# Performance work log

Measured on AMD Instinct MI355X. Metric: run time of the kernel, lower is better.

The kernel has to match this reference:

```python
import jax, jax.numpy as jnp
import numpy as np
import math

N_HEADS = 16
THETA = 10000.0


def setup_inputs() -> dict:
    key = jax.random.key(0)
    ks = jax.random.split(key, 5)
    B, T, D = 4, 2048, 1024
    return {
        "x": jax.random.normal(ks[0], (B, T, D), dtype=jnp.float32),
        "w_qkv": jax.random.normal(ks[1], (3 * D, D), dtype=jnp.float32) * 0.02,
        "b_qkv": jax.random.normal(ks[2], (3 * D,), dtype=jnp.float32) * 0.02,
        "w_out": jax.random.normal(ks[3], (D, D), dtype=jnp.float32) * 0.02,
        "b_out": jax.random.normal(ks[4], (D,), dtype=jnp.float32) * 0.02,
    }


def reference(x, w_qkv, b_qkv, w_out, b_out):
    B, T, D = x.shape
    H = N_HEADS
    hd = D // H
    half = hd // 2

    # fused QKV projection (nn.Linear: y = x @ W^T + b)
    qkv = (x @ w_qkv.T + b_qkv).reshape(B, T, 3, H, hd)
    q, k, v = qkv[:, :, 0], qkv[:, :, 1], qkv[:, :, 2]

    # RoPE: interleaved (even, odd) pairs treated as complex, rotated by e^{i t w}
    inv_freq = 1.0 / (THETA ** (jnp.arange(0, hd, 2, dtype=jnp.float32) / hd))  # [half]
    angles = jnp.arange(T, dtype=jnp.float32)[:, None] * inv_freq[None, :]      # [T, half]
    cos = jnp.cos(angles)[None, :, None, :]  # [1,T,1,half]
    sin = jnp.sin(angles)[None, :, None, :]

    def rotate(t):
        tr = t.reshape(B, T, H, half, 2)
        te, to = tr[..., 0], tr[..., 1]
        rot = jnp.stack([te * cos - to * sin, te * sin + to * cos], axis=-1)
        return rot.reshape(B, T, H, hd).astype(t.dtype)

    q, k = rotate(q), rotate(k)

    # non-causal SDPA, scale = 1/sqrt(head_dim)
    scale = 1.0 / math.sqrt(hd)
    scores = jnp.einsum("bqhd,bkhd->bhqk", q, k) * scale
    attn = jax.nn.softmax(scores, axis=-1)
    out = jnp.einsum("bhqk,bkhd->bqhd", attn, v).reshape(B, T, D)

    return out @ w_out.T + b_out
```

## Files before the change

### kernel.cpp

```cpp
#include <hip/hip_runtime.h>

typedef __attribute__((ext_vector_type(4))) float f32x4;
typedef __attribute__((ext_vector_type(16))) float f32x16;
typedef __attribute__((ext_vector_type(8))) short bf16x8;
typedef __attribute__((ext_vector_type(4))) unsigned u32x4;

__device__ __forceinline__ unsigned short f2bf(float f) {
  unsigned u = __float_as_uint(f);
  u += 0x7fff + ((u >> 16) & 1);
  return (unsigned short)(u >> 16);
}
__device__ __forceinline__ float bf2f(unsigned short h) {
  return __uint_as_float(((unsigned)h) << 16);
}

__device__ __forceinline__ void gload_lds16(const void* g, void* lds) {
  __builtin_amdgcn_global_load_lds(
      (const __attribute__((address_space(1))) unsigned int*)g,
      (__attribute__((address_space(3))) unsigned int*)lds, 16, 0, 0);
}

__global__ void cast_f32_bf16(const float* __restrict__ in,
                              unsigned short* __restrict__ out, int n4) {
  int i = blockIdx.x * blockDim.x + threadIdx.x;
  if (i >= n4) return;
  float4 v = ((const float4*)in)[i];
  ushort4 o;
  o.x = f2bf(v.x); o.y = f2bf(v.y); o.z = f2bf(v.z); o.w = f2bf(v.w);
  ((ushort4*)out)[i] = o;
}

__global__ void rope_table(float2* __restrict__ cs) {
  int idx = blockIdx.x * blockDim.x + threadIdx.x;
  if (idx >= 2048 * 32) return;
  int t = idx >> 5, i = idx & 31;
  float inv = powf(10000.0f, -(float)(2 * i) / 64.0f);
  float a = (float)t * inv;
  cs[idx] = make_float2(cosf(a), sinf(a));
}

__global__ void rope_apply_k(unsigned short* __restrict__ qkv,
                             const float2* __restrict__ cs) {
  int idx = blockIdx.x * blockDim.x + threadIdx.x;
  int i = idx & 31;
  int h = (idx >> 5) & 15;
  int t = (idx >> 9) & 2047;
  int b = idx >> 20;
  float2 v = cs[(t << 5) | i];
  unsigned short* p =
      qkv + ((size_t)((b << 11) + t)) * 3072 + 1024 + h * 64 + 2 * i;
  unsigned pr = *(unsigned*)p;
  float e = bf2f((unsigned short)(pr & 0xffff));
  float o = bf2f((unsigned short)(pr >> 16));
  float ne = e * v.x - o * v.y;
  float no = e * v.y + o * v.x;
  *(unsigned*)p = (unsigned)f2bf(ne) | ((unsigned)f2bf(no) << 16);
}

template <int OUT_BF16>
__global__ __launch_bounds__(256, 2) void gemm_bt(
    const unsigned short* __restrict__ A, const unsigned short* __restrict__ B,
    const float* __restrict__ bias, void* __restrict__ Cout,
    int M, int N, int K) {
  __shared__ unsigned short lA[128 * 64];
  __shared__ unsigned short lB[128 * 64];
  const int tiles_n = N >> 7;
  const int swz = (blockIdx.x & 7) * (gridDim.x >> 3) + (blockIdx.x >> 3);
  const int bm = swz / tiles_n;
  const int bn = swz % tiles_n;
  const int tid = threadIdx.x;
  const int w = tid >> 6, l = tid & 63;
  const int l15 = l & 15, lq = l >> 4;
  const int wm = (w >> 1) * 64, wn = (w & 1) * 64;
  const int m0 = bm << 7, n0 = bn << 7;
  const int arow = l >> 3;
  const int acol = (l & 7) * 8;
  f32x4 acc[4][4] = {};

  for (int k0 = 0; k0 < K; k0 += 64) {
    __syncthreads();
#pragma unroll
    for (int it = 0; it < 4; ++it) {
      const int rb = it * 32 + w * 8;
      gload_lds16(A + (size_t)(m0 + rb + arow) * K + k0 + acol, &lA[rb * 64]);
      gload_lds16(B + (size_t)(n0 + rb + arow) * K + k0 + acol, &lB[rb * 64]);
    }
    __syncthreads();
#pragma unroll
    for (int ks = 0; ks < 2; ++ks) {
      bf16x8 af[4], bfr[4];
#pragma unroll
      for (int mi = 0; mi < 4; ++mi)
        af[mi] = *(const bf16x8*)&lA[(wm + mi * 16 + l15) * 64 + ks * 32 + lq * 8];
#pragma unroll
      for (int ni = 0; ni < 4; ++ni)
        bfr[ni] = *(const bf16x8*)&lB[(wn + ni * 16 + l15) * 64 + ks * 32 + lq * 8];
#pragma unroll
      for (int mi = 0; mi < 4; ++mi)
#pragma unroll
        for (int ni = 0; ni < 4; ++ni)
          acc[mi][ni] = __builtin_amdgcn_mfma_f32_16x16x32_bf16(
              af[mi], bfr[ni], acc[mi][ni], 0, 0, 0);
    }
  }

#pragma unroll
  for (int ni = 0; ni < 4; ++ni) {
    const int c = n0 + wn + ni * 16 + l15;
    const float bv = bias[c];
#pragma unroll
    for (int mi = 0; mi < 4; ++mi) {
#pragma unroll
      for (int j = 0; j < 4; ++j) {
        const int r = m0 + wm + mi * 16 + lq * 4 + j;
        const float v = acc[mi][ni][j] + bv;
        if (OUT_BF16)
          ((unsigned short*)Cout)[(size_t)r * N + c] = f2bf(v);
        else
          ((float*)Cout)[(size_t)r * N + c] = v;
      }
    }
  }
}


#define PACKPV(SCV, KS)                                                        \
  do {                                                                         \
    unsigned xa, xb, ya, yb;                                                   \
    asm("v_cvt_pk_bf16_f32 %0, %1, %2"                                         \
        : "=v"(xa) : "v"(SCV[((KS) & 1) * 8 + 0]), "v"(SCV[((KS) & 1) * 8 + 1])); \
    asm("v_cvt_pk_bf16_f32 %0, %1, %2"                                         \
        : "=v"(xb) : "v"(SCV[((KS) & 1) * 8 + 2]), "v"(SCV[((KS) & 1) * 8 + 3])); \
    asm("v_cvt_pk_bf16_f32 %0, %1, %2"                                         \
        : "=v"(ya) : "v"(SCV[((KS) & 1) * 8 + 4]), "v"(SCV[((KS) & 1) * 8 + 5])); \
    asm("v_cvt_pk_bf16_f32 %0, %1, %2"                                         \
        : "=v"(yb) : "v"(SCV[((KS) & 1) * 8 + 6]), "v"(SCV[((KS) & 1) * 8 + 7])); \
    asm("v_permlane32_swap_b32 %0, %1" : "+v"(xa), "+v"(ya));                  \
    asm("v_permlane32_swap_b32 %0, %1" : "+v"(xb), "+v"(yb));                  \
    u32x4 pw;                                                                  \
    pw[0] = xa; pw[1] = xb; pw[2] = ya; pw[3] = yb;                            \
    const bf16x8 pa = __builtin_bit_cast(bf16x8, pw);                          \
    {                                                                          \
      const bf16x8 vf = *(const bf16x8*)                                       \
          &lVc[l31 * 136 + ((16 * (KS) + 8 * hi) ^ (l31 & 0x30))];             \
      o0 = __builtin_amdgcn_mfma_f32_32x32x16_bf16(pa, vf, o0, 0, 0, 0);       \
    }                                                                          \
    {                                                                          \
      const int vrow = 32 + l31;                                               \
      const bf16x8 vf = *(const bf16x8*)                                       \
          &lVc[vrow * 136 + ((16 * (KS) + 8 * hi) ^ (vrow & 0x30))];           \
      o1 = __builtin_amdgcn_mfma_f32_32x32x16_bf16(pa, vf, o1, 0, 0, 0);       \
    }                                                                          \
  } while (0)

__global__ __launch_bounds__(256, 2) void attn_fwd(
    const unsigned short* __restrict__ qkv, unsigned short* __restrict__ aout,
    const float2* __restrict__ cs) {
  __shared__ unsigned short lK[2 * 128 * 64];
  __shared__ unsigned short lVt[2 * 64 * 136];

  const int g = blockIdx.x;
  const int xcd = g & 7;
  const int j2 = g >> 3;
  const int bh = ((j2 >> 4) << 3) + xcd;
  const int qt = j2 & 15;
  const int h = bh & 15, b = bh >> 4;

  const int tid = threadIdx.x;
  const int w = tid >> 6, l = tid & 63;
  const int l31 = l & 31, hi = l >> 5;
  const int l7 = l & 7;

  const size_t bt_base = (size_t)(b * 2048) * 3072;
  const int qbase = qt * 128 + w * 32;

  const unsigned short* Qp =
      qkv + bt_base + (size_t)(qbase + l31) * 3072 + h * 64 + hi * 8;
  const float2* csrow = cs + (size_t)(qbase + l31) * 32;
  bf16x8 qf[4];
#pragma unroll
  for (int s = 0; s < 4; ++s) {
    bf16x8 q = *(const bf16x8*)(Qp + 16 * s);
#pragma unroll
    for (int j = 0; j < 4; ++j) {
      const float2 cn = csrow[8 * s + 4 * hi + j];
      const float e = bf2f((unsigned short)q[2 * j]);
      const float o = bf2f((unsigned short)q[2 * j + 1]);
      q[2 * j]     = (short)f2bf((e * cn.x - o * cn.y) * 0.125f);
      q[2 * j + 1] = (short)f2bf((e * cn.y + o * cn.x) * 0.125f);
    }
    qf[s] = q;
  }

  const unsigned short* Kp = qkv + bt_base + 1024 + h * 64;
  const unsigned short* Vp = qkv + bt_base + 2048 + h * 64;

  const int krow = l >> 3;
  const int kcol = ((l & 7) ^ (l >> 3)) << 3;

  const int vr = tid >> 2;
  const int vc0 = (tid & 3) << 4;

  f32x16 o0 = {}, o1 = {};
  float m_run = -1e30f, lsum = 0.f;
  bf16x8 v0, v1, v2, v3;
  const float L2E = 1.4426950408889634f;

  {
#pragma unroll
    for (int it = 0; it < 4; ++it) {
      const int rb = it * 32 + w * 8;
      gload_lds16(Kp + (size_t)(rb + krow) * 3072 + kcol, &lK[rb * 64]);
    }
    const unsigned short* vb = Vp + (size_t)vr * 3072 + vc0;
    v0 = *(const bf16x8*)vb;
    v1 = *(const bf16x8*)(vb + 8);
    const unsigned short* vb2 = vb + (size_t)64 * 3072;
    v2 = *(const bf16x8*)vb2;
    v3 = *(const bf16x8*)(vb2 + 8);
#pragma unroll
    for (int i2 = 0; i2 < 8; ++i2) {
      lVt[(vc0 + i2) * 136 + (vr ^ vc0)] = (unsigned short)v0[i2];
      lVt[(vc0 + 8 + i2) * 136 + (vr ^ vc0)] = (unsigned short)v1[i2];
      lVt[(vc0 + i2) * 136 + ((vr + 64) ^ vc0)] = (unsigned short)v2[i2];
      lVt[(vc0 + 8 + i2) * 136 + ((vr + 64) ^ vc0)] = (unsigned short)v3[i2];
    }
  }
  __syncthreads();

  for (int t = 0; t < 16; ++t) {
    const int cur = t & 1;
    const unsigned short* lKc = lK + cur * 8192;
    const unsigned short* lVc = lVt + cur * 8704;

    if (t < 15) {
      const unsigned short* kb = Kp + (size_t)(t + 1) * 128 * 3072;
      unsigned short* lKn = lK + (cur ^ 1) * 8192;
#pragma unroll
      for (int it = 0; it < 4; ++it) {
        const int rb = it * 32 + w * 8;
        gload_lds16(kb + (size_t)(rb + krow) * 3072 + kcol, lKn + rb * 64);
      }
      const unsigned short* vb =
          Vp + (size_t)(t + 1) * 128 * 3072 + (size_t)vr * 3072 + vc0;
      v0 = *(const bf16x8*)vb;
      v1 = *(const bf16x8*)(vb + 8);
      const unsigned short* vb2 = vb + (size_t)64 * 3072;
      v2 = *(const bf16x8*)vb2;
      v3 = *(const bf16x8*)(vb2 + 8);
    }

    f32x16 s0 = {}, s1 = {}, s2 = {}, s3 = {};
    __builtin_amdgcn_s_setprio(1);
#pragma unroll
    for (int s = 0; s < 4; ++s) {
      bf16x8 kf = *(const bf16x8*)&lKc[l31 * 64 + (((2 * s + hi) ^ l7) << 3)];
      s0 = __builtin_amdgcn_mfma_f32_32x32x16_bf16(kf, qf[s], s0, 0, 0, 0);
    }
#pragma unroll
    for (int s = 0; s < 4; ++s) {
      bf16x8 kf = *(const bf16x8*)&lKc[(32 + l31) * 64 + (((2 * s + hi) ^ l7) << 3)];
      s1 = __builtin_amdgcn_mfma_f32_32x32x16_bf16(kf, qf[s], s1, 0, 0, 0);
    }
#pragma unroll
    for (int s = 0; s < 4; ++s) {
      bf16x8 kf = *(const bf16x8*)&lKc[(64 + l31) * 64 + (((2 * s + hi) ^ l7) << 3)];
      s2 = __builtin_amdgcn_mfma_f32_32x32x16_bf16(kf, qf[s], s2, 0, 0, 0);
    }
#pragma unroll
    for (int s = 0; s < 4; ++s) {
      bf16x8 kf = *(const bf16x8*)&lKc[(96 + l31) * 64 + (((2 * s + hi) ^ l7) << 3)];
      s3 = __builtin_amdgcn_mfma_f32_32x32x16_bf16(kf, qf[s], s3, 0, 0, 0);
    }
    __builtin_amdgcn_s_setprio(0);

    {
      float pmax = -1e30f;
#pragma unroll
      for (int r = 0; r < 16; r += 2) {
        float t0, t1, t2, t3;
        asm("v_max3_f32 %0, %1, %2, %3"
            : "=v"(t0) : "v"(s0[r]), "v"(s0[r + 1]), "v"(pmax));
        asm("v_max3_f32 %0, %1, %2, %3"
            : "=v"(t1) : "v"(s1[r]), "v"(s1[r + 1]), "v"(t0));
        asm("v_max3_f32 %0, %1, %2, %3"
            : "=v"(t2) : "v"(s2[r]), "v"(s2[r + 1]), "v"(t1));
        asm("v_max3_f32 %0, %1, %2, %3"
            : "=v"(t3) : "v"(s3[r]), "v"(s3[r + 1]), "v"(t2));
        pmax = t3;
      }
      pmax = fmaxf(pmax, __shfl_xor(pmax, 32));
      if (!__all(pmax <= m_run + 8.0f)) {
        const float mn = fmaxf(m_run, pmax);
        const float alpha = __expf(m_run - mn);
        m_run = mn;
        lsum *= alpha;
#pragma unroll
        for (int r = 0; r < 16; ++r) {
          const float ar = __shfl(alpha, (r & 3) + 8 * (r >> 2) + 4 * hi);
          o0[r] *= ar;
          o1[r] *= ar;
        }
      }
      const float m2 = m_run * L2E;
      float rsa = 0.f, rsb = 0.f;
#pragma unroll
      for (int r = 0; r < 16; r += 2) {
        float a0 = __builtin_fmaf(s0[r], L2E, -m2);
        float a1 = __builtin_fmaf(s0[r + 1], L2E, -m2);
        float p0, p1;
        asm("v_exp_f32 %0, %1" : "=v"(p0) : "v"(a0));
        asm("v_exp_f32 %0, %1" : "=v"(p1) : "v"(a1));
        s0[r] = p0; s0[r + 1] = p1; rsa += p0; rsb += p1;
        a0 = __builtin_fmaf(s1[r], L2E, -m2);
        a1 = __builtin_fmaf(s1[r + 1], L2E, -m2);
        asm("v_exp_f32 %0, %1" : "=v"(p0) : "v"(a0));
        asm("v_exp_f32 %0, %1" : "=v"(p1) : "v"(a1));
        s1[r] = p0; s1[r + 1] = p1; rsa += p0; rsb += p1;
        a0 = __builtin_fmaf(s2[r], L2E, -m2);
        a1 = __builtin_fmaf(s2[r + 1], L2E, -m2);
        asm("v_exp_f32 %0, %1" : "=v"(p0) : "v"(a0));
        asm("v_exp_f32 %0, %1" : "=v"(p1) : "v"(a1));
        s2[r] = p0; s2[r + 1] = p1; rsa += p0; rsb += p1;
        a0 = __builtin_fmaf(s3[r], L2E, -m2);
        a1 = __builtin_fmaf(s3[r + 1], L2E, -m2);
        asm("v_exp_f32 %0, %1" : "=v"(p0) : "v"(a0));
        asm("v_exp_f32 %0, %1" : "=v"(p1) : "v"(a1));
        s3[r] = p0; s3[r + 1] = p1; rsa += p0; rsb += p1;
      }
      float rs = rsa + rsb;
      rs += __shfl_xor(rs, 32);
      lsum += rs;
    }

    __builtin_amdgcn_s_setprio(1);
    PACKPV(s0, 0);
    PACKPV(s0, 1);
    PACKPV(s1, 2);
    PACKPV(s1, 3);
    PACKPV(s2, 4);
    PACKPV(s2, 5);
    PACKPV(s3, 6);
    PACKPV(s3, 7);
    __builtin_amdgcn_s_setprio(0);

    if (t < 15) {
      unsigned short* lVn = lVt + (cur ^ 1) * 8704;
#pragma unroll
      for (int i2 = 0; i2 < 8; ++i2) {
        lVn[(vc0 + i2) * 136 + (vr ^ vc0)] = (unsigned short)v0[i2];
        lVn[(vc0 + 8 + i2) * 136 + (vr ^ vc0)] = (unsigned short)v1[i2];
        lVn[(vc0 + i2) * 136 + ((vr + 64) ^ vc0)] = (unsigned short)v2[i2];
        lVn[(vc0 + 8 + i2) * 136 + ((vr + 64) ^ vc0)] = (unsigned short)v3[i2];
      }
    }
    __syncthreads();
  }

  const float linv = 1.0f / lsum;
#pragma unroll
  for (int r = 0; r < 16; ++r) {
    const int crow = (r & 3) + 8 * (r >> 2) + 4 * hi;
    const float lr = __shfl(linv, crow);
    unsigned short* orow =
        aout + (size_t)(b * 2048 + qbase + crow) * 1024 + h * 64 + l31;
    orow[0] = f2bf(o0[r] * lr);
    orow[32] = f2bf(o1[r] * lr);
  }
}

extern "C" void kernel_launch(void* const* d_in, const int* in_sizes, int n_in,
                              void* d_out, int out_size, void* d_ws, size_t ws_size,
                              hipStream_t stream) {
  const float* x     = (const float*)d_in[0];
  const float* w_qkv = (const float*)d_in[1];
  const float* b_qkv = (const float*)d_in[2];
  const float* w_out = (const float*)d_in[3];
  const float* b_out = (const float*)d_in[4];
  float* out = (float*)d_out;

  char* ws = (char*)d_ws;
  unsigned short* x_bf    = (unsigned short*)(ws);
  unsigned short* wqkv_bf = (unsigned short*)(ws + 16777216);
  unsigned short* wout_bf = (unsigned short*)(ws + 23068672);
  unsigned short* qkv     = (unsigned short*)(ws + 25165824);
  unsigned short* aout    = (unsigned short*)(ws + 75497472);
  float2* cs              = (float2*)(ws + 92274688);

  cast_f32_bf16<<<2097152 / 256, 256, 0, stream>>>(x, x_bf, 2097152);
  cast_f32_bf16<<<786432 / 256, 256, 0, stream>>>(w_qkv, wqkv_bf, 786432);
  cast_f32_bf16<<<262144 / 256, 256, 0, stream>>>(w_out, wout_bf, 262144);
  rope_table<<<65536 / 256, 256, 0, stream>>>(cs);

  gemm_bt<1><<<64 * 24, 256, 0, stream>>>(x_bf, wqkv_bf, b_qkv, qkv,
                                          8192, 3072, 1024);
  rope_apply_k<<<4194304 / 256, 256, 0, stream>>>(qkv, cs);
  attn_fwd<<<1024, 256, 0, stream>>>(qkv, aout, cs);
  gemm_bt<0><<<64 * 8, 256, 0, stream>>>(aout, wout_bf, b_out, out,
                                         8192, 1024, 1024);
}
```

Baseline: 219.9 us.

## Use 512-thread attention blocks with 64-key tiles; fuse three cast kernels

The attention kernel now runs 8 waves per block over 256 query rows and iterates over 64-key K/V tiles (32 iterations) instead of 4 waves with 128-key tiles. This halves the LDS footprint per block and doubles the number of waves sharing each K/V tile, aiming for more reuse and occupancy. The cost is twice as many barriers and a shorter compute span per iteration to hide the next tile's loads behind. Separately, the three f32-to-bf16 cast launches are merged into one kernel that branches on index range, removing two launches.

```diff
diff --git a/kernel.cpp b/kernel.cpp
--- a/kernel.cpp
+++ b/kernel.cpp
@@ -20,14 +20,23 @@
       (__attribute__((address_space(3))) unsigned int*)lds, 16, 0, 0);
 }
 
-__global__ void cast_f32_bf16(const float* __restrict__ in,
-                              unsigned short* __restrict__ out, int n4) {
+__global__ void cast3_f32_bf16(const float* __restrict__ x,
+                               const float* __restrict__ wq,
+                               const float* __restrict__ wo,
+                               unsigned short* __restrict__ xb,
+                               unsigned short* __restrict__ wqb,
+                               unsigned short* __restrict__ wob) {
   int i = blockIdx.x * blockDim.x + threadIdx.x;
-  if (i >= n4) return;
-  float4 v = ((const float4*)in)[i];
+  const float* src;
+  unsigned short* dst;
+  int off;
+  if (i < 2097152) { src = x;  dst = xb;  off = i; }
+  else if (i < 2883584) { src = wq; dst = wqb; off = i - 2097152; }
+  else { src = wo; dst = wob; off = i - 2883584; }
+  float4 v = ((const float4*)src)[off];
   ushort4 o;
   o.x = f2bf(v.x); o.y = f2bf(v.y); o.z = f2bf(v.z); o.w = f2bf(v.w);
-  ((ushort4*)out)[i] = o;
+  ((ushort4*)dst)[off] = o;
 }
 
 __global__ void rope_table(float2* __restrict__ cs) {
@@ -142,28 +151,28 @@
     const bf16x8 pa = __builtin_bit_cast(bf16x8, pw);                          \
     {                                                                          \
       const bf16x8 vf = *(const bf16x8*)                                       \
-          &lVc[l31 * 136 + ((16 * (KS) + 8 * hi) ^ (l31 & 0x30))];             \
+          &lVc[l31 * 72 + ((16 * (KS) + 8 * hi) ^ (l31 & 0x30))];              \
       o0 = __builtin_amdgcn_mfma_f32_32x32x16_bf16(pa, vf, o0, 0, 0, 0);       \
     }                                                                          \
     {                                                                          \
       const int vrow = 32 + l31;                                               \
       const bf16x8 vf = *(const bf16x8*)                                       \
-          &lVc[vrow * 136 + ((16 * (KS) + 8 * hi) ^ (vrow & 0x30))];           \
+          &lVc[vrow * 72 + ((16 * (KS) + 8 * hi) ^ (vrow & 0x30))];            \
       o1 = __builtin_amdgcn_mfma_f32_32x32x16_bf16(pa, vf, o1, 0, 0, 0);       \
     }                                                                          \
   } while (0)
 
-__global__ __launch_bounds__(256, 2) void attn_fwd(
+__global__ __launch_bounds__(512, 4) void attn_fwd(
     const unsigned short* __restrict__ qkv, unsigned short* __restrict__ aout,
     const float2* __restrict__ cs) {
-  __shared__ unsigned short lK[2 * 128 * 64];
-  __shared__ unsigned short lVt[2 * 64 * 136];
+  __shared__ unsigned short lK[2 * 64 * 64];
+  __shared__ unsigned short lVt[2 * 64 * 72];
 
   const int g = blockIdx.x;
   const int xcd = g & 7;
   const int j2 = g >> 3;
-  const int bh = ((j2 >> 4) << 3) + xcd;
-  const int qt = j2 & 15;
+  const int bh = ((j2 >> 3) << 3) + xcd;
+  const int qt = j2 & 7;
   const int h = bh & 15, b = bh >> 4;
 
   const int tid = threadIdx.x;
@@ -172,7 +181,7 @@
   const int l7 = l & 7;
 
   const size_t bt_base = (size_t)(b * 2048) * 3072;
-  const int qbase = qt * 128 + w * 32;
+  const int qbase = qt * 256 + w * 32;
 
   const unsigned short* Qp =
       qkv + bt_base + (size_t)(qbase + l31) * 3072 + h * 64 + hi * 8;
@@ -198,59 +207,39 @@
   const int krow = l >> 3;
   const int kcol = ((l & 7) ^ (l >> 3)) << 3;
 
-  const int vr = tid >> 2;
-  const int vc0 = (tid & 3) << 4;
+  const int vr = tid >> 3;
+  const int vc0 = (tid & 7) << 3;
+  const int vx = vc0 & 0x30;
 
   f32x16 o0 = {}, o1 = {};
   float m_run = -1e30f, lsum = 0.f;
-  bf16x8 v0, v1, v2, v3;
+  bf16x8 v0;
   const float L2E = 1.4426950408889634f;
 
   {
-#pragma unroll
-    for (int it = 0; it < 4; ++it) {
-      const int rb = it * 32 + w * 8;
-      gload_lds16(Kp + (size_t)(rb + krow) * 3072 + kcol, &lK[rb * 64]);
-    }
+    gload_lds16(Kp + (size_t)(w * 8 + krow) * 3072 + kcol, &lK[(w * 8) * 64]);
     const unsigned short* vb = Vp + (size_t)vr * 3072 + vc0;
     v0 = *(const bf16x8*)vb;
-    v1 = *(const bf16x8*)(vb + 8);
-    const unsigned short* vb2 = vb + (size_t)64 * 3072;
-    v2 = *(const bf16x8*)vb2;
-    v3 = *(const bf16x8*)(vb2 + 8);
-#pragma unroll
-    for (int i2 = 0; i2 < 8; ++i2) {
-      lVt[(vc0 + i2) * 136 + (vr ^ vc0)] = (unsigned short)v0[i2];
-      lVt[(vc0 + 8 + i2) * 136 + (vr ^ vc0)] = (unsigned short)v1[i2];
-      lVt[(vc0 + i2) * 136 + ((vr + 64) ^ vc0)] = (unsigned short)v2[i2];
-      lVt[(vc0 + 8 + i2) * 136 + ((vr + 64) ^ vc0)] = (unsigned short)v3[i2];
-    }
   }
   __syncthreads();
-
-  for (int t = 0; t < 16; ++t) {
+#pragma unroll
+  for (int i2 = 0; i2 < 8; ++i2)
+    lVt[(vc0 + i2) * 72 + (vr ^ vx)] = (unsigned short)v0[i2];
+  __syncthreads();
+
+  for (int t = 0; t < 32; ++t) {
     const int cur = t & 1;
-    const unsigned short* lKc = lK + cur * 8192;
-    const unsigned short* lVc = lVt + cur * 8704;
-
-    if (t < 15) {
-      const unsigned short* kb = Kp + (size_t)(t + 1) * 128 * 3072;
-      unsigned short* lKn = lK + (cur ^ 1) * 8192;
-#pragma unroll
-      for (int it = 0; it < 4; ++it) {
-        const int rb = it * 32 + w * 8;
-        gload_lds16(kb + (size_t)(rb + krow) * 3072 + kcol, lKn + rb * 64);
-      }
-      const unsigned short* vb =
-          Vp + (size_t)(t + 1) * 128 * 3072 + (size_t)vr * 3072 + vc0;
-      v0 = *(const bf16x8*)vb;
-      v1 = *(const bf16x8*)(vb + 8);
-      const unsigned short* vb2 = vb + (size_t)64 * 3072;
-      v2 = *(const bf16x8*)vb2;
-      v3 = *(const bf16x8*)(vb2 + 8);
-    }
-
-    f32x16 s0 = {}, s1 = {}, s2 = {}, s3 = {};
+    const unsigned short* lKc = lK + cur * 4096;
+    const unsigned short* lVc = lVt + cur * 4608;
+    const bool stage = (t < 31);
+
+    if (stage) {
+      const unsigned short* kb = Kp + (size_t)(t + 1) * 64 * 3072;
+      gload_lds16(kb + (size_t)(w * 8 + krow) * 3072 + kcol,
+                  lK + (cur ^ 1) * 4096 + (w * 8) * 64);
+    }
+
+    f32x16 s0 = {}, s1 = {};
     __builtin_amdgcn_s_setprio(1);
 #pragma unroll
     for (int s = 0; s < 4; ++s) {
@@ -262,32 +251,24 @@
       bf16x8 kf = *(const bf16x8*)&lKc[(32 + l31) * 64 + (((2 * s + hi) ^ l7) << 3)];
       s1 = __builtin_amdgcn_mfma_f32_32x32x16_bf16(kf, qf[s], s1, 0, 0, 0);
     }
-#pragma unroll
-    for (int s = 0; s < 4; ++s) {
-      bf16x8 kf = *(const bf16x8*)&lKc[(64 + l31) * 64 + (((2 * s + hi) ^ l7) << 3)];
-      s2 = __builtin_amdgcn_mfma_f32_32x32x16_bf16(kf, qf[s], s2, 0, 0, 0);
-    }
-#pragma unroll
-    for (int s = 0; s < 4; ++s) {
-      bf16x8 kf = *(const bf16x8*)&lKc[(96 + l31) * 64 + (((2 * s + hi) ^ l7) << 3)];
-      s3 = __builtin_amdgcn_mfma_f32_32x32x16_bf16(kf, qf[s], s3, 0, 0, 0);
-    }
     __builtin_amdgcn_s_setprio(0);
+
+    if (stage) {
+      const unsigned short* vb =
+          Vp + (size_t)(t + 1) * 64 * 3072 + (size_t)vr * 3072 + vc0;
+      v0 = *(const bf16x8*)vb;
+    }
 
     {
       float pmax = -1e30f;
 #pragma unroll
       for (int r = 0; r < 16; r += 2) {
-        float t0, t1, t2, t3;
+        float t0, t1;
         asm("v_max3_f32 %0, %1, %2, %3"
             : "=v"(t0) : "v"(s0[r]), "v"(s0[r + 1]), "v"(pmax));
         asm("v_max3_f32 %0, %1, %2, %3"
             : "=v"(t1) : "v"(s1[r]), "v"(s1[r + 1]), "v"(t0));
-        asm("v_max3_f32 %0, %1, %2, %3"
-            : "=v"(t2) : "v"(s2[r]), "v"(s2[r + 1]), "v"(t1));
-        asm("v_max3_f32 %0, %1, %2, %3"
-            : "=v"(t3) : "v"(s3[r]), "v"(s3[r + 1]), "v"(t2));
-        pmax = t3;
+        pmax = t1;
       }
       pmax = fmaxf(pmax, __shfl_xor(pmax, 32));
       if (!__all(pmax <= m_run + 8.0f)) {
@@ -317,16 +298,6 @@
         asm("v_exp_f32 %0, %1" : "=v"(p0) : "v"(a0));
         asm("v_exp_f32 %0, %1" : "=v"(p1) : "v"(a1));
         s1[r] = p0; s1[r + 1] = p1; rsa += p0; rsb += p1;
-        a0 = __builtin_fmaf(s2[r], L2E, -m2);
-        a1 = __builtin_fmaf(s2[r + 1], L2E, -m2);
-        asm("v_exp_f32 %0, %1" : "=v"(p0) : "v"(a0));
-        asm("v_exp_f32 %0, %1" : "=v"(p1) : "v"(a1));
-        s2[r] = p0; s2[r + 1] = p1; rsa += p0; rsb += p1;
-        a0 = __builtin_fmaf(s3[r], L2E, -m2);
-        a1 = __builtin_fmaf(s3[r + 1], L2E, -m2);
-        asm("v_exp_f32 %0, %1" : "=v"(p0) : "v"(a0));
-        asm("v_exp_f32 %0, %1" : "=v"(p1) : "v"(a1));
-        s3[r] = p0; s3[r + 1] = p1; rsa += p0; rsb += p1;
       }
       float rs = rsa + rsb;
       rs += __shfl_xor(rs, 32);
@@ -338,21 +309,13 @@
     PACKPV(s0, 1);
     PACKPV(s1, 2);
     PACKPV(s1, 3);
-    PACKPV(s2, 4);
-    PACKPV(s2, 5);
-    PACKPV(s3, 6);
-    PACKPV(s3, 7);
     __builtin_amdgcn_s_setprio(0);
 
-    if (t < 15) {
-      unsigned short* lVn = lVt + (cur ^ 1) * 8704;
-#pragma unroll
-      for (int i2 = 0; i2 < 8; ++i2) {
-        lVn[(vc0 + i2) * 136 + (vr ^ vc0)] = (unsigned short)v0[i2];
-        lVn[(vc0 + 8 + i2) * 136 + (vr ^ vc0)] = (unsigned short)v1[i2];
-        lVn[(vc0 + i2) * 136 + ((vr + 64) ^ vc0)] = (unsigned short)v2[i2];
-        lVn[(vc0 + 8 + i2) * 136 + ((vr + 64) ^ vc0)] = (unsigned short)v3[i2];
-      }
+    if (stage) {
+      unsigned short* lVn = lVt + (cur ^ 1) * 4608;
+#pragma unroll
+      for (int i2 = 0; i2 < 8; ++i2)
+        lVn[(vc0 + i2) * 72 + (vr ^ vx)] = (unsigned short)v0[i2];
     }
     __syncthreads();
   }
@@ -387,15 +350,14 @@
   unsigned short* aout    = (unsigned short*)(ws + 75497472);
   float2* cs              = (float2*)(ws + 92274688);
 
-  cast_f32_bf16<<<2097152 / 256, 256, 0, stream>>>(x, x_bf, 2097152);
-  cast_f32_bf16<<<786432 / 256, 256, 0, stream>>>(w_qkv, wqkv_bf, 786432);
-  cast_f32_bf16<<<262144 / 256, 256, 0, stream>>>(w_out, wout_bf, 262144);
+  cast3_f32_bf16<<<3145728 / 256, 256, 0, stream>>>(x, w_qkv, w_out,
+                                                    x_bf, wqkv_bf, wout_bf);
   rope_table<<<65536 / 256, 256, 0, stream>>>(cs);
 
   gemm_bt<1><<<64 * 24, 256, 0, stream>>>(x_bf, wqkv_bf, b_qkv, qkv,
                                           8192, 3072, 1024);
   rope_apply_k<<<4194304 / 256, 256, 0, stream>>>(qkv, cs);
-  attn_fwd<<<1024, 256, 0, stream>>>(qkv, aout, cs);
+  attn_fwd<<<512, 512, 0, stream>>>(qkv, aout, cs);
   gemm_bt<0><<<64 * 8, 256, 0, stream>>>(aout, wout_bf, b_out, out,
                                          8192, 1024, 1024);
 }
```

New measurement: 209.9 us. -4.5%, faster.
